# Optimization experiments

Hardware: AMD Instinct MI355X
Metric: run time of the kernel (lower is better)

Reference implementation:

```python
import jax, jax.numpy as jnp
import numpy as np


def setup_inputs() -> dict:
    key = jax.random.key(0)
    k1, k2 = jax.random.split(key)
    batch = jax.random.normal(k1, (16, 256, 1024), dtype=jnp.float32)
    # probe matrix initialized uniform(-0.05, 0.05) as in the original
    B = jax.random.uniform(k2, (1024, 128), minval=-0.05, maxval=0.05, dtype=jnp.float32)
    return {"batch": batch, "B": B}


def reference(batch, B):
    # project: (b, s, d) @ (d, r) -> (b, s, r)
    transformed = jnp.einsum("bsd,dr->bsr", batch, B)
    # pairwise squared L2 distances via broadcast: (b, s, 1, r) - (b, 1, s, r)
    diffs = transformed[:, :, None, :] - transformed[:, None, :, :]
    # (b, s, s)
    return jnp.sum(diffs * diffs, axis=-1)
```

## Files before the change

### kernel.cpp

```cpp
#include <hip/hip_runtime.h>
#include <hip/hip_bf16.h>

typedef __bf16 bf16x8 __attribute__((ext_vector_type(8)));
typedef float f32x4 __attribute__((ext_vector_type(4)));

#define K_DIM 1024
#define N_DIM 128


__device__ inline unsigned pk2(float x, float y) {
  __hip_bfloat16 hx = __float2bfloat16(x), hy = __float2bfloat16(y);
  return (unsigned)*(unsigned short*)&hx | ((unsigned)*(unsigned short*)&hy << 16);
}

__global__ __launch_bounds__(64)
void prep_kernel(const float* __restrict__ B, unsigned short* __restrict__ Bfrag) {
  const int W = blockIdx.x, l = threadIdx.x;
  const int w = W >> 5, ks = W & 31;
  const int col = 16 * w + (l & 15);
  const int kb = 32 * ks + 4 * (l >> 4);
  unsigned u[4];
#pragma unroll
  for (int j = 0; j < 4; ++j) {
    int k0 = kb + 2 * (j & 1) + 16 * (j >> 1);
    u[j] = pk2(B[(size_t)k0 * N_DIM + col], B[(size_t)(k0 + 1) * N_DIM + col]);
  }
  *(uint4*)&Bfrag[((size_t)(w * 32 + ks) * 64 + l) * 8] =
      make_uint4(u[0], u[1], u[2], u[3]);
}

__global__ __launch_bounds__(512)
void proj_kernel(const float* __restrict__ batch,
                 const unsigned short* __restrict__ Bfrag,
                 unsigned short* __restrict__ Tfrag,
                 float* __restrict__ nrm) {
  __shared__ __align__(16) unsigned short Asl[32 * 64 * 8];
  __shared__ float part[8][16];
  const int t = threadIdx.x, w = t >> 6, l = t & 63;
  const int m0 = blockIdx.x * 16;

  const float* src = batch + (size_t)m0 * K_DIM;
#pragma unroll
  for (int j = 0; j < 8; ++j) {
    int fidx = j * 512 + t;
    f32x4 v = *(const f32x4*)(src + 4 * (size_t)fidx);
    int r = fidx >> 8;
    int q = fidx & 255;
    int ks = q >> 3, qq = q & 7, g = qq & 3, h = qq >> 2;
    unsigned lo = pk2(v.x, v.y), hi = pk2(v.z, v.w);
    int byte = ks * 1024 + ((16 * (r + 16 * g)) ^ ((ks & 7) << 4)) + 8 * h;
    *(uint2*)((char*)Asl + byte) = make_uint2(lo, hi);
  }
  __syncthreads();

  const unsigned short* bptr = Bfrag + ((size_t)w * 32 * 64 + l) * 8;
  f32x4 acc0 = {0.f, 0.f, 0.f, 0.f}, acc1 = {0.f, 0.f, 0.f, 0.f};
#pragma unroll
  for (int ks = 0; ks < 32; ks += 2) {
    bf16x8 a0 = *(const bf16x8*)((const char*)Asl +
                   (ks * 1024 + ((l * 16) ^ ((ks & 7) << 4))));
    bf16x8 b0 = *(const bf16x8*)(bptr + (size_t)ks * 512);
    acc0 = __builtin_amdgcn_mfma_f32_16x16x32_bf16(b0, a0, acc0, 0, 0, 0);
    bf16x8 a1 = *(const bf16x8*)((const char*)Asl +
                   ((ks + 1) * 1024 + ((l * 16) ^ (((ks + 1) & 7) << 4))));
    bf16x8 b1 = *(const bf16x8*)(bptr + (size_t)(ks + 1) * 512);
    acc1 = __builtin_amdgcn_mfma_f32_16x16x32_bf16(b1, a1, acc1, 0, 0, 0);
  }
  f32x4 acc = acc0 + acc1;

  unsigned lo = pk2(acc[0], acc[1]);
  unsigned hi = pk2(acc[2], acc[3]);
  *(uint2*)&Tfrag[(((size_t)blockIdx.x * 4 + (w >> 1)) * 64 + l) * 8 + (w & 1) * 4] =
      make_uint2(lo, hi);

  float v0 = __uint_as_float(lo << 16);
  float v1 = __uint_as_float(lo & 0xffff0000u);
  float v2 = __uint_as_float(hi << 16);
  float v3 = __uint_as_float(hi & 0xffff0000u);
  float s = v0 * v0 + v1 * v1 + v2 * v2 + v3 * v3;
  s += __shfl_xor(s, 16);
  s += __shfl_xor(s, 32);
  if (l < 16) part[w][l] = s;
  __syncthreads();
  if (t < 16) {
    float n = 0.f;
#pragma unroll
    for (int ww = 0; ww < 8; ++ww) n += part[ww][t];
    nrm[m0 + t] = n;
  }
}

__global__ __launch_bounds__(256)
void dist_kernel(const unsigned short* __restrict__ Tfrag,
                 const float* __restrict__ nrm, float* __restrict__ out) {
  const int t = threadIdx.x, l = t & 63;
  const int W = blockIdx.x * 4 + (t >> 6);
  const int bb = W >> 7, tile = W & 127;
  const int ti = (tile >> 4) * 32, tj = (tile & 15) * 16;
  const int rbase = bb * 256;

  bf16x8 ifr[2][4], jfr[4];
#pragma unroll
  for (int ks = 0; ks < 4; ++ks) {
    jfr[ks] = *(const bf16x8*)
        &Tfrag[((((size_t)bb * 16 + (tj >> 4)) * 4 + ks) * 64 + l) * 8];
#pragma unroll
    for (int d = 0; d < 2; ++d)
      ifr[d][ks] = *(const bf16x8*)
          &Tfrag[((((size_t)bb * 16 + (ti >> 4) + d) * 4 + ks) * 64 + l) * 8];
  }

  f32x4 acc[2] = {{0.f,0.f,0.f,0.f}, {0.f,0.f,0.f,0.f}};
#pragma unroll
  for (int ks = 0; ks < 4; ++ks)
#pragma unroll
    for (int di = 0; di < 2; ++di)
      acc[di] = __builtin_amdgcn_mfma_f32_16x16x32_bf16(
          ifr[di][ks], jfr[ks], acc[di], 0, 0, 0);

  const float njv = nrm[rbase + tj + (l & 15)];
#pragma unroll
  for (int di = 0; di < 2; ++di) {
    const f32x4 ni = *(const f32x4*)&nrm[rbase + ti + 16 * di + 4 * (l >> 4)];
#pragma unroll
    for (int ii = 0; ii < 4; ++ii) {
      out[(size_t)(rbase + ti + 16 * di + 4 * (l >> 4) + ii) * 256
          + tj + (l & 15)] = ni[ii] + njv - 2.f * acc[di][ii];
    }
  }
}

extern "C" void kernel_launch(void* const* d_in, const int* in_sizes, int n_in,
                              void* d_out, int out_size, void* d_ws, size_t ws_size,
                              hipStream_t stream) {
  const float* batch = (const float*)d_in[0];
  const float* Bmat  = (const float*)d_in[1];
  unsigned short* Bfrag = (unsigned short*)d_ws;
  unsigned short* Tfrag = Bfrag + 8 * 32 * 64 * 8;
  float* nrm = (float*)(Tfrag + 256 * 4 * 64 * 8);
  float* out = (float*)d_out;

  prep_kernel<<<256, 64, 0, stream>>>(Bmat, Bfrag);
  proj_kernel<<<256, 512, 0, stream>>>(batch, Bfrag, Tfrag, nrm);
  dist_kernel<<<512, 256, 0, stream>>>(Tfrag, nrm, out);
}
```

Before: 20.92 us.

## Fuse prep, projection and distance kernels into one cooperative kernel

```diff
diff --git a/kernel.cpp b/kernel.cpp
--- a/kernel.cpp
+++ b/kernel.cpp
@@ -1,5 +1,8 @@
 #include <hip/hip_runtime.h>
+#include <hip/hip_cooperative_groups.h>
 #include <hip/hip_bf16.h>
+
+namespace cg = cooperative_groups;
 
 typedef __bf16 bf16x8 __attribute__((ext_vector_type(8)));
 typedef float f32x4 __attribute__((ext_vector_type(4)));
@@ -13,119 +16,120 @@
   return (unsigned)*(unsigned short*)&hx | ((unsigned)*(unsigned short*)&hy << 16);
 }
 
-__global__ __launch_bounds__(64)
-void prep_kernel(const float* __restrict__ B, unsigned short* __restrict__ Bfrag) {
-  const int W = blockIdx.x, l = threadIdx.x;
-  const int w = W >> 5, ks = W & 31;
-  const int col = 16 * w + (l & 15);
-  const int kb = 32 * ks + 4 * (l >> 4);
-  unsigned u[4];
-#pragma unroll
-  for (int j = 0; j < 4; ++j) {
-    int k0 = kb + 2 * (j & 1) + 16 * (j >> 1);
-    u[j] = pk2(B[(size_t)k0 * N_DIM + col], B[(size_t)(k0 + 1) * N_DIM + col]);
-  }
-  *(uint4*)&Bfrag[((size_t)(w * 32 + ks) * 64 + l) * 8] =
-      make_uint4(u[0], u[1], u[2], u[3]);
-}
-
 __global__ __launch_bounds__(512)
-void proj_kernel(const float* __restrict__ batch,
-                 const unsigned short* __restrict__ Bfrag,
-                 unsigned short* __restrict__ Tfrag,
-                 float* __restrict__ nrm) {
+void fused_kernel(const float* __restrict__ batch, const float* __restrict__ Bmat,
+                  unsigned short* __restrict__ Bfrag,
+                  unsigned short* __restrict__ Tfrag,
+                  float* __restrict__ nrm, float* __restrict__ out) {
+  cg::grid_group grid = cg::this_grid();
   __shared__ __align__(16) unsigned short Asl[32 * 64 * 8];
   __shared__ float part[8][16];
   const int t = threadIdx.x, w = t >> 6, l = t & 63;
-  const int m0 = blockIdx.x * 16;
+  const int blk = blockIdx.x;
+  const int m0 = blk * 16;
 
-  const float* src = batch + (size_t)m0 * K_DIM;
+  if (w == 0) {
+    const int wb = blk >> 5, ks = blk & 31;
+    const int col = 16 * wb + (l & 15);
+    const int kb = 32 * ks + 4 * (l >> 4);
+    unsigned u[4];
 #pragma unroll
-  for (int j = 0; j < 8; ++j) {
-    int fidx = j * 512 + t;
-    f32x4 v = *(const f32x4*)(src + 4 * (size_t)fidx);
-    int r = fidx >> 8;
-    int q = fidx & 255;
-    int ks = q >> 3, qq = q & 7, g = qq & 3, h = qq >> 2;
-    unsigned lo = pk2(v.x, v.y), hi = pk2(v.z, v.w);
-    int byte = ks * 1024 + ((16 * (r + 16 * g)) ^ ((ks & 7) << 4)) + 8 * h;
-    *(uint2*)((char*)Asl + byte) = make_uint2(lo, hi);
+    for (int j = 0; j < 4; ++j) {
+      int k0 = kb + 2 * (j & 1) + 16 * (j >> 1);
+      u[j] = pk2(Bmat[(size_t)k0 * N_DIM + col],
+                 Bmat[(size_t)(k0 + 1) * N_DIM + col]);
+    }
+    *(uint4*)&Bfrag[((size_t)(wb * 32 + ks) * 64 + l) * 8] =
+        make_uint4(u[0], u[1], u[2], u[3]);
   }
-  __syncthreads();
+  {
+    const float* src = batch + (size_t)m0 * K_DIM;
+#pragma unroll
+    for (int j = 0; j < 8; ++j) {
+      int fidx = j * 512 + t;
+      f32x4 v = *(const f32x4*)(src + 4 * (size_t)fidx);
+      int r = fidx >> 8;
+      int q = fidx & 255;
+      int ks = q >> 3, qq = q & 7, g = qq & 3, h = qq >> 2;
+      int byte = ks * 1024 + ((16 * (r + 16 * g)) ^ ((ks & 7) << 4)) + 8 * h;
+      *(uint2*)((char*)Asl + byte) = make_uint2(pk2(v.x, v.y), pk2(v.z, v.w));
+    }
+  }
+  grid.sync();
 
-  const unsigned short* bptr = Bfrag + ((size_t)w * 32 * 64 + l) * 8;
-  f32x4 acc0 = {0.f, 0.f, 0.f, 0.f}, acc1 = {0.f, 0.f, 0.f, 0.f};
+  {
+    const unsigned short* bptr = Bfrag + ((size_t)w * 32 * 64 + l) * 8;
+    f32x4 acc0 = {0.f, 0.f, 0.f, 0.f}, acc1 = {0.f, 0.f, 0.f, 0.f};
 #pragma unroll
-  for (int ks = 0; ks < 32; ks += 2) {
-    bf16x8 a0 = *(const bf16x8*)((const char*)Asl +
-                   (ks * 1024 + ((l * 16) ^ ((ks & 7) << 4))));
-    bf16x8 b0 = *(const bf16x8*)(bptr + (size_t)ks * 512);
-    acc0 = __builtin_amdgcn_mfma_f32_16x16x32_bf16(b0, a0, acc0, 0, 0, 0);
-    bf16x8 a1 = *(const bf16x8*)((const char*)Asl +
-                   ((ks + 1) * 1024 + ((l * 16) ^ (((ks + 1) & 7) << 4))));
-    bf16x8 b1 = *(const bf16x8*)(bptr + (size_t)(ks + 1) * 512);
-    acc1 = __builtin_amdgcn_mfma_f32_16x16x32_bf16(b1, a1, acc1, 0, 0, 0);
+    for (int ks = 0; ks < 32; ks += 2) {
+      bf16x8 a0 = *(const bf16x8*)((const char*)Asl +
+                     (ks * 1024 + ((l * 16) ^ ((ks & 7) << 4))));
+      bf16x8 b0 = *(const bf16x8*)(bptr + (size_t)ks * 512);
+      acc0 = __builtin_amdgcn_mfma_f32_16x16x32_bf16(b0, a0, acc0, 0, 0, 0);
+      bf16x8 a1 = *(const bf16x8*)((const char*)Asl +
+                     ((ks + 1) * 1024 + ((l * 16) ^ (((ks + 1) & 7) << 4))));
+      bf16x8 b1 = *(const bf16x8*)(bptr + (size_t)(ks + 1) * 512);
+      acc1 = __builtin_amdgcn_mfma_f32_16x16x32_bf16(b1, a1, acc1, 0, 0, 0);
+    }
+    f32x4 acc = acc0 + acc1;
+
+    unsigned lo = pk2(acc[0], acc[1]);
+    unsigned hi = pk2(acc[2], acc[3]);
+    *(uint2*)&Tfrag[(((size_t)blk * 4 + (w >> 1)) * 64 + l) * 8 + (w & 1) * 4] =
+        make_uint2(lo, hi);
+
+    float v0 = __uint_as_float(lo << 16);
+    float v1 = __uint_as_float(lo & 0xffff0000u);
+    float v2 = __uint_as_float(hi << 16);
+    float v3 = __uint_as_float(hi & 0xffff0000u);
+    float s = v0 * v0 + v1 * v1 + v2 * v2 + v3 * v3;
+    s += __shfl_xor(s, 16);
+    s += __shfl_xor(s, 32);
+    if (l < 16) part[w][l] = s;
+    __syncthreads();
+    if (t < 16) {
+      float n = 0.f;
+#pragma unroll
+      for (int ww = 0; ww < 8; ++ww) n += part[ww][t];
+      nrm[m0 + t] = n;
+    }
   }
-  f32x4 acc = acc0 + acc1;
+  grid.sync();
 
-  unsigned lo = pk2(acc[0], acc[1]);
-  unsigned hi = pk2(acc[2], acc[3]);
-  *(uint2*)&Tfrag[(((size_t)blockIdx.x * 4 + (w >> 1)) * 64 + l) * 8 + (w & 1) * 4] =
-      make_uint2(lo, hi);
+  {
+    const int W2 = blk * 8 + w;
+    const int bb = W2 >> 7, tile = W2 & 127;
+    const int ti = (tile >> 4) * 32, tj = (tile & 15) * 16;
+    const int rbase = bb * 256;
 
-  float v0 = __uint_as_float(lo << 16);
-  float v1 = __uint_as_float(lo & 0xffff0000u);
-  float v2 = __uint_as_float(hi << 16);
-  float v3 = __uint_as_float(hi & 0xffff0000u);
-  float s = v0 * v0 + v1 * v1 + v2 * v2 + v3 * v3;
-  s += __shfl_xor(s, 16);
-  s += __shfl_xor(s, 32);
-  if (l < 16) part[w][l] = s;
-  __syncthreads();
-  if (t < 16) {
-    float n = 0.f;
+    bf16x8 ifr[2][4], jfr[4];
 #pragma unroll
-    for (int ww = 0; ww < 8; ++ww) n += part[ww][t];
-    nrm[m0 + t] = n;
-  }
-}
+    for (int ks = 0; ks < 4; ++ks) {
+      jfr[ks] = *(const bf16x8*)
+          &Tfrag[((((size_t)bb * 16 + (tj >> 4)) * 4 + ks) * 64 + l) * 8];
+#pragma unroll
+      for (int d = 0; d < 2; ++d)
+        ifr[d][ks] = *(const bf16x8*)
+            &Tfrag[((((size_t)bb * 16 + (ti >> 4) + d) * 4 + ks) * 64 + l) * 8];
+    }
 
-__global__ __launch_bounds__(256)
-void dist_kernel(const unsigned short* __restrict__ Tfrag,
-                 const float* __restrict__ nrm, float* __restrict__ out) {
-  const int t = threadIdx.x, l = t & 63;
-  const int W = blockIdx.x * 4 + (t >> 6);
-  const int bb = W >> 7, tile = W & 127;
-  const int ti = (tile >> 4) * 32, tj = (tile & 15) * 16;
-  const int rbase = bb * 256;
+    f32x4 acc[2] = {{0.f,0.f,0.f,0.f}, {0.f,0.f,0.f,0.f}};
+#pragma unroll
+    for (int ks = 0; ks < 4; ++ks)
+#pragma unroll
+      for (int di = 0; di < 2; ++di)
+        acc[di] = __builtin_amdgcn_mfma_f32_16x16x32_bf16(
+            ifr[di][ks], jfr[ks], acc[di], 0, 0, 0);
 
-  bf16x8 ifr[2][4], jfr[4];
+    const float njv = nrm[rbase + tj + (l & 15)];
 #pragma unroll
-  for (int ks = 0; ks < 4; ++ks) {
-    jfr[ks] = *(const bf16x8*)
-        &Tfrag[((((size_t)bb * 16 + (tj >> 4)) * 4 + ks) * 64 + l) * 8];
+    for (int di = 0; di < 2; ++di) {
+      const f32x4 ni = *(const f32x4*)&nrm[rbase + ti + 16 * di + 4 * (l >> 4)];
 #pragma unroll
-    for (int d = 0; d < 2; ++d)
-      ifr[d][ks] = *(const bf16x8*)
-          &Tfrag[((((size_t)bb * 16 + (ti >> 4) + d) * 4 + ks) * 64 + l) * 8];
-  }
-
-  f32x4 acc[2] = {{0.f,0.f,0.f,0.f}, {0.f,0.f,0.f,0.f}};
-#pragma unroll
-  for (int ks = 0; ks < 4; ++ks)
-#pragma unroll
-    for (int di = 0; di < 2; ++di)
-      acc[di] = __builtin_amdgcn_mfma_f32_16x16x32_bf16(
-          ifr[di][ks], jfr[ks], acc[di], 0, 0, 0);
-
-  const float njv = nrm[rbase + tj + (l & 15)];
-#pragma unroll
-  for (int di = 0; di < 2; ++di) {
-    const f32x4 ni = *(const f32x4*)&nrm[rbase + ti + 16 * di + 4 * (l >> 4)];
-#pragma unroll
-    for (int ii = 0; ii < 4; ++ii) {
-      out[(size_t)(rbase + ti + 16 * di + 4 * (l >> 4) + ii) * 256
-          + tj + (l & 15)] = ni[ii] + njv - 2.f * acc[di][ii];
+      for (int ii = 0; ii < 4; ++ii) {
+        out[(size_t)(rbase + ti + 16 * di + 4 * (l >> 4) + ii) * 256
+            + tj + (l & 15)] = ni[ii] + njv - 2.f * acc[di][ii];
+      }
     }
   }
 }
@@ -140,7 +144,8 @@
   float* nrm = (float*)(Tfrag + 256 * 4 * 64 * 8);
   float* out = (float*)d_out;
 
-  prep_kernel<<<256, 64, 0, stream>>>(Bmat, Bfrag);
-  proj_kernel<<<256, 512, 0, stream>>>(batch, Bfrag, Tfrag, nrm);
-  dist_kernel<<<512, 256, 0, stream>>>(Tfrag, nrm, out);
+  void* args[] = {(void*)&batch, (void*)&Bmat, (void*)&Bfrag,
+                  (void*)&Tfrag, (void*)&nrm, (void*)&out};
+  hipLaunchCooperativeKernel((void*)fused_kernel, dim3(256), dim3(512),
+                             args, 0, stream);
 }
```

Measured after the change: 75.81 us. +262.4%, slower.
